# Kernel optimization log

Hardware: AMD Instinct MI355X
Metric: run time of the kernel (lower is better)

Reference implementation:

```python
import jax, jax.numpy as jnp
import numpy as np

LAYERS = [2, 1024, 512, 256, 128, 1]
LB = jnp.array([0.0, 0.0], dtype=jnp.float32)
UB = jnp.array([2.0 * np.pi, 1.0], dtype=jnp.float32)


def _block_diag_mask(num_blocks, bs1, bs2):
    return jnp.kron(jnp.eye(num_blocks, dtype=jnp.float32), jnp.ones((bs1, bs2), jnp.float32))


def _masks():
    # masks for l in range(2, num_Layers - 2) with num_Layers = len(LAYERS) = 6 -> l in {2, 3}
    width = [LAYERS[0]] + [(2 ** (i - 1)) * LAYERS[i] for i in range(1, len(LAYERS) - 1)] + [LAYERS[-1]]
    masks = []
    for l in range(2, len(LAYERS) - 2):
        num_blocks = 2 ** (l - 1)
        bs1 = width[l] // num_blocks
        bs2 = 2 * LAYERS[l + 1]
        masks.append(_block_diag_mask(num_blocks, bs1, bs2))
    return masks


def setup_inputs() -> dict:
    key = jax.random.key(0)
    ks = jax.random.split(key, 8)
    N = 65536
    H = 1024

    def xavier(k, fi, fo):
        lim = float(np.sqrt(6.0 / (fi + fo)))
        return jax.random.uniform(k, (fi, fo), jnp.float32, -lim, lim)

    X = jax.random.uniform(ks[0], (N, 2), jnp.float32, 0.0, 1.0) * (UB - LB) + LB
    return {
        "X": X,
        "W0": xavier(ks[1], 2, H), "b0": jnp.zeros((1, H), jnp.float32),
        "W1": xavier(ks[2], H, H), "b1": jnp.zeros((1, H), jnp.float32),
        "W2": xavier(ks[3], H, H), "b2": jnp.zeros((1, H), jnp.float32),
        "W3": xavier(ks[4], H, H), "b3": jnp.zeros((1, H), jnp.float32),
        "W_last": xavier(ks[5], H, 1), "b_last": jnp.zeros((1, 1), jnp.float32),
    }


def reference(X, W0, b0, W1, b1, W2, b2, W3, b3, W_last, b_last):
    mask2, mask3 = _masks()
    # input normalization to [-1, 1]
    h = 2.0 * (X - LB) / (UB - LB) - 1.0
    h = jnp.tanh(h @ W0 + b0)                 # layer 0: dense
    h = jnp.tanh(h @ W1 + b1)                 # layer 1: dense (no mask in forward)
    h = jnp.tanh(h @ (W2 * mask2) + b2)       # layer 2: block-diagonal masked
    h = jnp.tanh(h @ (W3 * mask3) + b3)       # layer 3: block-diagonal masked
    return h @ W_last + b_last                # output layer, [N, 1]
```

## Files before the change

### kernel.cpp

```cpp
#include <hip/hip_runtime.h>
#include <cstdint>
#include <cstddef>


typedef _Float16  f16x8   __attribute__((ext_vector_type(8)));
typedef float     floatx4 __attribute__((ext_vector_type(4)));
typedef float     floatx8 __attribute__((ext_vector_type(8)));

__device__ __forceinline__ float tanh_fast(float x) {
    float e = __expf(2.0f * x);
    return 1.0f - 2.0f / (e + 1.0f);
}

__global__ __launch_bounds__(256)
void transposeH3(const float* __restrict__ W1, const float* __restrict__ W2,
                 const float* __restrict__ W3, _Float16* __restrict__ Wt1,
                 _Float16* __restrict__ Wt2, _Float16* __restrict__ Wt3) {
    const float* W = blockIdx.z == 0 ? W1 : (blockIdx.z == 1 ? W2 : W3);
    _Float16* Wt   = blockIdx.z == 0 ? Wt1 : (blockIdx.z == 1 ? Wt2 : Wt3);
    __shared__ float tile[32][33];
    const int tx = threadIdx.x & 31;
    const int ty = threadIdx.x >> 5;
    #pragma unroll
    for (int j = 0; j < 4; ++j) {
        int r = ty + j * 8;
        tile[r][tx] = W[(size_t)(blockIdx.y * 32 + r) * 1024 + blockIdx.x * 32 + tx];
    }
    __syncthreads();
    #pragma unroll
    for (int j = 0; j < 4; ++j) {
        int r = ty + j * 8;
        Wt[(size_t)(blockIdx.x * 32 + r) * 1024 + blockIdx.y * 32 + tx] =
            (_Float16)tile[tx][r];
    }
}

__global__ __launch_bounds__(256)
void init_out(float* __restrict__ out, const float* __restrict__ bl) {
    out[blockIdx.x * 256 + threadIdx.x] = bl[0];
}

__global__ __launch_bounds__(256)
void layer0_kernel(const float* __restrict__ X, const float* __restrict__ W0,
                   const float* __restrict__ b0, _Float16* __restrict__ H) {
    const int idx = blockIdx.x * 256 + threadIdx.x;
    const int row = idx >> 7;
    const int j0  = (idx & 127) << 3;
    const float x0 = X[row * 2 + 0];
    const float x1 = X[row * 2 + 1];
    const float xa = x0 * 0.31830988618379067f - 1.0f;
    const float xb = 2.0f * x1 - 1.0f;
    floatx8 wa = *(const floatx8*)(W0 + j0);
    floatx8 wb = *(const floatx8*)(W0 + 1024 + j0);
    floatx8 bb = *(const floatx8*)(b0 + j0);
    f16x8 o;
    #pragma unroll
    for (int j = 0; j < 8; ++j) {
        float v = fmaf(xa, wa[j], fmaf(xb, wb[j], bb[j]));
        o[j] = (_Float16)tanh_fast(v);
    }
    *(f16x8*)(H + (size_t)row * 1024 + j0) = o;
}

template <bool FUSE>
__global__ __launch_bounds__(320)
void gemm_tanh_f16(const _Float16* __restrict__ A, const _Float16* __restrict__ Bt,
                   const float* __restrict__ bias, _Float16* __restrict__ C,
                   const float* __restrict__ Wl, float* __restrict__ out, int KB) {
    __shared__ _Float16 lds[2][8192];

    const int tid  = threadIdx.x;
    const int lane = tid & 63;
    const int wave = tid >> 6;
    const int m0 = blockIdx.x * 128;
    const int n0 = blockIdx.y * 128;
    const int kbeg   = (n0 / KB) * KB;
    const int kiters = KB >> 5;

    if (wave == 4) {
        const int row0 = lane >> 2;
        const int sg   = (lane & 3) << 3;
        const size_t gaBase = (size_t)(m0 + row0) * 1024 + kbeg + sg;
        const size_t gbBase = (size_t)(n0 + row0) * 1024 + kbeg + sg;
        const int lsBase = lane * 8;
        f16x8 ra[8], rb[8];
        #pragma unroll
        for (int i = 0; i < 8; ++i) {
            ra[i] = *(const f16x8*)(A + gaBase + (size_t)i * 16384);
            rb[i] = *(const f16x8*)(Bt + gbBase + (size_t)i * 16384);
        }
        #pragma unroll
        for (int i = 0; i < 8; ++i) {
            *(f16x8*)(&lds[0][lsBase + i * 512]) = ra[i];
            *(f16x8*)(&lds[0][4096 + lsBase + i * 512]) = rb[i];
        }
        __syncthreads();
        for (int t = 0; t < kiters; ++t) {
            if (t + 1 < kiters) {
                const size_t d = (size_t)(t + 1) << 5;
                #pragma unroll
                for (int i = 0; i < 8; ++i) {
                    ra[i] = *(const f16x8*)(A + gaBase + (size_t)i * 16384 + d);
                    rb[i] = *(const f16x8*)(Bt + gbBase + (size_t)i * 16384 + d);
                }
                _Float16* dst = lds[(t + 1) & 1];
                #pragma unroll
                for (int i = 0; i < 8; ++i) {
                    *(f16x8*)(dst + lsBase + i * 512) = ra[i];
                    *(f16x8*)(dst + 4096 + lsBase + i * 512) = rb[i];
                }
            }
            __syncthreads();
        }
        return;
    }

    const int wm = (wave & 1) << 6;
    const int wn = (wave >> 1) << 6;
    const int r = lane & 15;
    const int q = lane >> 4;

    floatx4 acc[4][4];
    #pragma unroll
    for (int i = 0; i < 4; ++i)
        #pragma unroll
        for (int j = 0; j < 4; ++j)
            acc[i][j] = floatx4{0.f, 0.f, 0.f, 0.f};

    __syncthreads();
    for (int t = 0; t < kiters; ++t) {
        const _Float16* As = lds[t & 1];
        const _Float16* Bs = As + 4096;
        f16x8 af[4], bf[4];
        #pragma unroll
        for (int i = 0; i < 4; ++i) {
            af[i] = *(const f16x8*)(As + (wm + i * 16 + r) * 32 + q * 8);
            bf[i] = *(const f16x8*)(Bs + (wn + i * 16 + r) * 32 + q * 8);
        }
        #pragma unroll
        for (int i = 0; i < 4; ++i)
            #pragma unroll
            for (int j = 0; j < 4; ++j)
                acc[i][j] = __builtin_amdgcn_mfma_f32_16x16x32_f16(af[i], bf[j], acc[i][j], 0, 0, 0);
        __syncthreads();
    }

    float bv[4], wlv[4];
    #pragma unroll
    for (int j = 0; j < 4; ++j) {
        const int col = n0 + wn + j * 16 + r;
        bv[j] = bias[col];
        if (FUSE) wlv[j] = Wl[col];
    }
    #pragma unroll
    for (int i = 0; i < 4; ++i) {
        const int row0 = m0 + wm + i * 16 + q * 4;
        #pragma unroll
        for (int rr = 0; rr < 4; ++rr) {
            if (!FUSE) {
                #pragma unroll
                for (int j = 0; j < 4; ++j) {
                    float o = tanh_fast(acc[i][j][rr] + bv[j]);
                    const int col = n0 + wn + j * 16 + r;
                    C[(size_t)(row0 + rr) * 1024 + col] = (_Float16)o;
                }
            } else {
                float p = 0.f;
                #pragma unroll
                for (int j = 0; j < 4; ++j)
                    p = fmaf(tanh_fast(acc[i][j][rr] + bv[j]), wlv[j], p);
                p += __shfl_down(p, 8);
                p += __shfl_down(p, 4);
                p += __shfl_down(p, 2);
                p += __shfl_down(p, 1);
                if (r == 0) atomicAdd(out + row0 + rr, p);
            }
        }
    }
}

extern "C" void kernel_launch(void* const* d_in, const int* in_sizes, int n_in,
                              void* d_out, int out_size, void* d_ws, size_t ws_size,
                              hipStream_t stream) {
    const float* X  = (const float*)d_in[0];
    const float* W0 = (const float*)d_in[1];
    const float* b0 = (const float*)d_in[2];
    const float* W1 = (const float*)d_in[3];
    const float* b1 = (const float*)d_in[4];
    const float* W2 = (const float*)d_in[5];
    const float* b2 = (const float*)d_in[6];
    const float* W3 = (const float*)d_in[7];
    const float* b3 = (const float*)d_in[8];
    const float* Wl = (const float*)d_in[9];
    const float* bl = (const float*)d_in[10];
    float* out = (float*)d_out;

    const int Nrows = in_sizes[0] / 2;
    const size_t WT = 1024 * 1024;
    const size_t wt_bytes = 3 * WT * 2;
    const size_t slack = 512;

    int R = 0;
    const int Rcap = Nrows < 32768 ? Nrows : 32768;
    for (int r = Rcap; r >= 256; r >>= 1)
        if ((size_t)2 * r * 2048 + wt_bytes + slack <= ws_size) { R = r; break; }
    if (!R) return;

    _Float16* wsp = (_Float16*)d_ws;
    _Float16* Wt1 = wsp;
    _Float16* Wt2 = Wt1 + WT;
    _Float16* Wt3 = Wt2 + WT;
    const size_t plane = (size_t)R * 1024;
    _Float16* P0 = Wt3 + WT;
    _Float16* P1 = P0 + plane;

    const dim3 tb(256);
    transposeH3<<<dim3(32, 32, 3), tb, 0, stream>>>(W1, W2, W3, Wt1, Wt2, Wt3);
    init_out<<<Nrows / 256, tb, 0, stream>>>(out, bl);

    const int nchunks = Nrows / R;
    for (int c = 0; c < nchunks; ++c) {
        const float* Xc = X + (size_t)c * R * 2;
        float* outc = out + (size_t)c * R;

        layer0_kernel<<<R / 2, tb, 0, stream>>>(Xc, W0, b0, P0);

        const dim3 tg(320);
        const dim3 gg(R / 128, 8);
        gemm_tanh_f16<false><<<gg, tg, 0, stream>>>(P0, Wt1, b1, P1, nullptr, nullptr, 1024);
        gemm_tanh_f16<false><<<gg, tg, 0, stream>>>(P1, Wt2, b2, P0, nullptr, nullptr, 512);
        gemm_tanh_f16<true ><<<gg, tg, 0, stream>>>(P0, Wt3, b3, nullptr, Wl, outc, 256);
    }
}
```

Baseline: 584.5 us.

## Triple-buffer LDS in producer wave and prefetch global loads two steps ahead

```diff
diff --git a/kernel.cpp b/kernel.cpp
--- a/kernel.cpp
+++ b/kernel.cpp
@@ -67,7 +67,7 @@
 void gemm_tanh_f16(const _Float16* __restrict__ A, const _Float16* __restrict__ Bt,
                    const float* __restrict__ bias, _Float16* __restrict__ C,
                    const float* __restrict__ Wl, float* __restrict__ out, int KB) {
-    __shared__ _Float16 lds[2][8192];
+    __shared__ _Float16 lds[3][8192];
 
     const int tid  = threadIdx.x;
     const int lane = tid & 63;
@@ -80,37 +80,50 @@
     if (wave == 4) {
         const int row0 = lane >> 2;
         const int sg   = (lane & 3) << 3;
-        const size_t gaBase = (size_t)(m0 + row0) * 1024 + kbeg + sg;
-        const size_t gbBase = (size_t)(n0 + row0) * 1024 + kbeg + sg;
-        const int lsBase = lane * 8;
-        f16x8 ra[8], rb[8];
+        const _Float16* pA = A  + (size_t)(m0 + row0) * 1024 + kbeg + sg;
+        const _Float16* pB = Bt + (size_t)(n0 + row0) * 1024 + kbeg + sg;
+        const int ls = lane * 8;
+        f16x8 rA[8], rB[8];
         #pragma unroll
         for (int i = 0; i < 8; ++i) {
-            ra[i] = *(const f16x8*)(A + gaBase + (size_t)i * 16384);
-            rb[i] = *(const f16x8*)(Bt + gbBase + (size_t)i * 16384);
+            rA[i] = *(const f16x8*)(pA + (size_t)i * 16384);
+            rB[i] = *(const f16x8*)(pB + (size_t)i * 16384);
         }
         #pragma unroll
         for (int i = 0; i < 8; ++i) {
-            *(f16x8*)(&lds[0][lsBase + i * 512]) = ra[i];
-            *(f16x8*)(&lds[0][4096 + lsBase + i * 512]) = rb[i];
-        }
-        __syncthreads();
+            *(f16x8*)(&lds[0][ls + i * 512]) = rA[i];
+            *(f16x8*)(&lds[0][4096 + ls + i * 512]) = rB[i];
+        }
+        if (kiters > 1) {
+            #pragma unroll
+            for (int i = 0; i < 8; ++i) {
+                rA[i] = *(const f16x8*)(pA + (size_t)i * 16384 + 32);
+                rB[i] = *(const f16x8*)(pB + (size_t)i * 16384 + 32);
+            }
+        }
+        asm volatile("s_waitcnt lgkmcnt(0)" ::: "memory");
+        asm volatile("s_barrier" ::: "memory");
+        int widx = 1;
         for (int t = 0; t < kiters; ++t) {
             if (t + 1 < kiters) {
-                const size_t d = (size_t)(t + 1) << 5;
+                _Float16* dst = &lds[widx][0];
+                widx = (widx == 2) ? 0 : widx + 1;
                 #pragma unroll
                 for (int i = 0; i < 8; ++i) {
-                    ra[i] = *(const f16x8*)(A + gaBase + (size_t)i * 16384 + d);
-                    rb[i] = *(const f16x8*)(Bt + gbBase + (size_t)i * 16384 + d);
+                    *(f16x8*)(dst + ls + i * 512) = rA[i];
+                    *(f16x8*)(dst + 4096 + ls + i * 512) = rB[i];
                 }
-                _Float16* dst = lds[(t + 1) & 1];
-                #pragma unroll
-                for (int i = 0; i < 8; ++i) {
-                    *(f16x8*)(dst + lsBase + i * 512) = ra[i];
-                    *(f16x8*)(dst + 4096 + lsBase + i * 512) = rb[i];
+                if (t + 2 < kiters) {
+                    const size_t d = (size_t)(t + 2) << 5;
+                    #pragma unroll
+                    for (int i = 0; i < 8; ++i) {
+                        rA[i] = *(const f16x8*)(pA + (size_t)i * 16384 + d);
+                        rB[i] = *(const f16x8*)(pB + (size_t)i * 16384 + d);
+                    }
                 }
+                asm volatile("s_waitcnt lgkmcnt(0)" ::: "memory");
             }
-            __syncthreads();
+            asm volatile("s_barrier" ::: "memory");
         }
         return;
     }
@@ -128,9 +141,11 @@
             acc[i][j] = floatx4{0.f, 0.f, 0.f, 0.f};
 
     __syncthreads();
+    int ridx = 0;
     for (int t = 0; t < kiters; ++t) {
-        const _Float16* As = lds[t & 1];
+        const _Float16* As = &lds[ridx][0];
         const _Float16* Bs = As + 4096;
+        ridx = (ridx == 2) ? 0 : ridx + 1;
         f16x8 af[4], bf[4];
         #pragma unroll
         for (int i = 0; i < 4; ++i) {
```

New measurement: 616.6 us. 1.05x slower.
